# Performance work log

Measured on AMD Instinct MI355X. Metric: run time of the kernel, lower is better.

## Reference

```python
import jax, jax.numpy as jnp
import numpy as np

EMB = 1024
HEAD = 64
RANK = 8
LRA_SCL = 2.0
LORA = 1.0


def setup_inputs() -> dict:
    key = jax.random.key(0)
    ks = jax.random.split(key, 12)
    s = 1.0 / np.sqrt(EMB)
    sr = 1.0 / np.sqrt(RANK)
    inp = {
        "batEmb": jax.random.normal(ks[0], (8, 2048, EMB), dtype=jnp.float32),
        "tokMrk": jax.random.randint(ks[1], (8, 2048), 0, 2, dtype=jnp.int32),
        # base projections, nn.Linear weight layout [out, in]
        "Wq": jax.random.uniform(ks[2], (HEAD, EMB), jnp.float32, -s, s),
        "Wk": jax.random.uniform(ks[3], (HEAD, EMB), jnp.float32, -s, s),
        "Wv": jax.random.uniform(ks[4], (HEAD, EMB), jnp.float32, -s, s),
        # LoRA: A [rank, emb], B [head, rank]. (Original inits B to zero; we
        # randomize with small scale so the LoRA path is numerically exercised.)
        "Aq": jax.random.uniform(ks[5], (RANK, EMB), jnp.float32, -s, s),
        "Bq": jax.random.uniform(ks[6], (HEAD, RANK), jnp.float32, -sr, sr) * 0.02,
        "Ak": jax.random.uniform(ks[7], (RANK, EMB), jnp.float32, -s, s),
        "Bk": jax.random.uniform(ks[8], (HEAD, RANK), jnp.float32, -sr, sr) * 0.02,
        "Av": jax.random.uniform(ks[9], (RANK, EMB), jnp.float32, -s, s),
        "Bv": jax.random.uniform(ks[10], (HEAD, RANK), jnp.float32, -sr, sr) * 0.02,
    }
    return inp


def _proj(x, W, A, B):
    # base + LoRA low-rank delta (dropout = identity in eval)
    base = jnp.einsum('bse,he->bsh', x, W)
    lora = jnp.einsum('bsr,hr->bsh', jnp.einsum('bse,re->bsr', x, A), B)
    return base + lora * (LRA_SCL * LORA)


def reference(batEmb, tokMrk, Wq, Wk, Wv, Aq, Bq, Ak, Bk, Av, Bv):
    q = _proj(batEmb, Wq, Aq, Bq)  # [B,S,H]
    k = _proj(batEmb, Wk, Ak, Bk)
    v = _proj(batEmb, Wv, Av, Bv)
    w = jnp.einsum('bqh,bkh->bqk', q, k) * (HEAD ** -0.5)  # [B,S,S]
    mask = (tokMrk == 0)[:, None, :]  # [B,1,S] over key dim
    w = jnp.where(mask, -jnp.inf, w)
    w = jax.nn.softmax(w, axis=-1)
    w = jnp.nan_to_num(w, nan=0.0)
    return jnp.einsum('bqk,bkh->bqh', w, v)
```

## Files before the change

### kernel.cpp

```cpp
#include <hip/hip_runtime.h>
#include <hip/hip_bf16.h>
#include <stdint.h>

#define EMB 1024
#define NB 8
#define SEQ 2048
#define RANK 8
#define SPLIT 4

#define BM 32
#define BK 64
#define NSTG 16
#define XBUF 8192
#define WBUF 24576

#define QSCL 0.180336880f

typedef __attribute__((ext_vector_type(8))) short bf16x8;
typedef __attribute__((ext_vector_type(4))) float f32x4;
typedef unsigned short u16;
typedef unsigned int u32;

__device__ __forceinline__ u16 f2bf(float f) {
  u32 u = __builtin_bit_cast(u32, f);
  u = (u + 0x7fffu + ((u >> 16) & 1u)) >> 16;
  return (u16)u;
}
__device__ __forceinline__ u32 pk2(float lo, float hi) {
  return (u32)f2bf(lo) | ((u32)f2bf(hi) << 16);
}
__device__ __forceinline__ u32 cvtpk(float lo, float hi) {
  __hip_bfloat162 h = __float22bfloat162_rn(make_float2(lo, hi));
  u32 u; __builtin_memcpy(&u, &h, 4); return u;
}
__device__ __forceinline__ void gll16(const void* g, void* l) {
  __builtin_amdgcn_global_load_lds(
      (const __attribute__((address_space(1))) unsigned int*)g,
      (__attribute__((address_space(3))) unsigned int*)l, 16, 0, 0);
}

#define PBAR()   asm volatile("s_barrier" ::: "memory")
#define WAITV(n) asm volatile("s_waitcnt vmcnt(" #n ")" ::: "memory")

__global__ __launch_bounds__(256) void fold_k(
    const float* __restrict__ Wq, const float* __restrict__ Wk, const float* __restrict__ Wv,
    const float* __restrict__ Aq, const float* __restrict__ Bq,
    const float* __restrict__ Ak, const float* __restrict__ Bk,
    const float* __restrict__ Av, const float* __restrict__ Bv,
    u16* __restrict__ weff) {
  int m = blockIdx.x;
  int mat = m >> 6, h = m & 63;
  const float* W = mat == 0 ? Wq : (mat == 1 ? Wk : Wv);
  const float* A = mat == 0 ? Aq : (mat == 1 ? Ak : Av);
  const float* B = mat == 0 ? Bq : (mat == 1 ? Bk : Bv);
  float bb[RANK];
#pragma unroll
  for (int r = 0; r < RANK; r++) bb[r] = 2.0f * B[h * RANK + r];
  int e = threadIdx.x * 4;
  float4 w4 = *(const float4*)(W + h * EMB + e);
  float a0 = w4.x, a1 = w4.y, a2 = w4.z, a3 = w4.w;
#pragma unroll
  for (int r = 0; r < RANK; r++) {
    float4 av = *(const float4*)(A + r * EMB + e);
    a0 += bb[r] * av.x; a1 += bb[r] * av.y; a2 += bb[r] * av.z; a3 += bb[r] * av.w;
  }
  u16* o = weff + (size_t)m * EMB + e;
  o[0] = f2bf(a0); o[1] = f2bf(a1); o[2] = f2bf(a2); o[3] = f2bf(a3);
}

__global__ __launch_bounds__(320) void proj_k(
    const float* __restrict__ X, const u16* __restrict__ weff,
    u16* __restrict__ qws, u16* __restrict__ kws, u16* __restrict__ vws) {
  extern __shared__ __align__(16) char smem[];
  char* xsm = smem;
  char* wsm = smem + 3 * XBUF;

  int t = threadIdx.x;
  int w = t >> 6, l = t & 63;
  int rbase = blockIdx.x * BM;

  if (w >= 3) {
    int q = w - 3;
    int lr4 = l >> 4;
    int l15 = l & 15;
    int wc0 = l >> 3;
    int wkoff = ((l & 7) ^ wc0) * 8;

#define ISSUE_X(st, bufp) do {                                                 \
    _Pragma("unroll")                                                          \
    for (int i_ = 0; i_ < 4; i_++) {                                           \
      int rrel_ = q * 16 + i_ * 4 + lr4;                                       \
      int xo_ = 4 * (l15 ^ (rrel_ & 7));        \
      gll16(X + (size_t)(rbase + rrel_) * EMB + (st) * BK + xo_,               \
            (bufp) + q * 4096 + i_ * 1024);                                    \
    } } while (0)

#define ISSUE_W(st, bufp) do {                                                 \
    _Pragma("unroll")                                                          \
    for (int i_ = 0; i_ < 12; i_++) { int wj_ = q * 12 + i_;                   \
      gll16(weff + (size_t)(wj_ * 8 + wc0) * EMB + (st) * BK + wkoff,          \
            (bufp) + wj_ * 1024);                                              \
    } } while (0)

    ISSUE_W(0, wsm);
    ISSUE_X(0, xsm);
    ISSUE_X(1, xsm + XBUF);
    WAITV(4);
    PBAR();
    for (int s = 0; s < NSTG; s++) {
      if (s + 1 < NSTG) ISSUE_W(s + 1, wsm + ((s + 1) & 1) * WBUF);
      if (s + 2 < NSTG) ISSUE_X(s + 2, xsm + ((s + 2) % 3) * XBUF);
      if (s + 1 < NSTG) {
        if (s + 2 < NSTG) { WAITV(4); } else { WAITV(0); }
        PBAR();
      }
    }
#undef ISSUE_X
#undef ISSUE_W
  } else {
    int l15 = l & 15, lh = l >> 4;
    f32x4 acc[2][4];
    f32x4 zero = {0.f, 0.f, 0.f, 0.f};
#pragma unroll
    for (int rt = 0; rt < 2; rt++)
#pragma unroll
      for (int ct = 0; ct < 4; ct++) acc[rt][ct] = zero;

    for (int s = 0; s < NSTG; s++) {
      PBAR();
      const char* bx = xsm + (s % 3) * XBUF;
      const char* bw = wsm + (s & 1) * WBUF;
#pragma unroll
      for (int j = 0; j < 2; j++) {
        bf16x8 a[2];
#pragma unroll
        for (int rt = 0; rt < 2; rt++) {
          int r = rt * 16 + l15;
          int sw = (r & 7) << 4;
          const char* base = bx + r * 256;
          f32x4 lo = *(const f32x4*)(base + ((j * 128 + lh * 32) ^ sw));
          f32x4 hi = *(const f32x4*)(base + ((j * 128 + lh * 32 + 16) ^ sw));
          union { bf16x8 v; u32 u[4]; } au;
          au.u[0] = cvtpk(lo.x, lo.y); au.u[1] = cvtpk(lo.z, lo.w);
          au.u[2] = cvtpk(hi.x, hi.y); au.u[3] = cvtpk(hi.z, hi.w);
          a[rt] = au.v;
        }
        __builtin_amdgcn_s_setprio(1);
#pragma unroll
        for (int ct = 0; ct < 4; ct++) {
          int col = w * 64 + ct * 16 + l15;
          bf16x8 bf = *(const bf16x8*)(bw + col * 128 +
                                       ((j * 64 + lh * 16) ^ ((col & 7) << 4)));
#pragma unroll
          for (int rt = 0; rt < 2; rt++)
            acc[rt][ct] = __builtin_amdgcn_mfma_f32_16x16x32_bf16(a[rt], bf, acc[rt][ct], 0, 0, 0);
        }
        __builtin_amdgcn_s_setprio(0);
      }
    }

#pragma unroll
    for (int rt = 0; rt < 2; rt++)
#pragma unroll
      for (int ct = 0; ct < 4; ct++) {
        int c = w * 64 + ct * 16 + l15;
#pragma unroll
        for (int r = 0; r < 4; r++) {
          int rr = rbase + rt * 16 + lh * 4 + r;
          float av = acc[rt][ct][r];
          if (c < 64) av *= QSCL;
          u16 v = f2bf(av);
          if (c < 64) {
            qws[(size_t)rr * 64 + c] = v;
          } else if (c < 128) {
            kws[(size_t)rr * 64 + (c - 64)] = v;
          } else {
            int bb = rr >> 11, tok = rr & 2047;
            vws[((size_t)(bb * 64 + (c - 128))) * SEQ + tok] = v;
          }
        }
      }
  }
}

__global__ __launch_bounds__(256) void attn_k(
    const u16* __restrict__ qws, const u16* __restrict__ kws, const u16* __restrict__ vws,
    const int* __restrict__ mrk,
    float* __restrict__ po, float* __restrict__ pmp, float* __restrict__ plp) {
  __shared__ __align__(16) u16 ks[2 * 4096];
  __shared__ __align__(16) u16 vt[2 * 4096];
  __shared__ __align__(16) u16 ps[4 * 1024];
  __shared__ __align__(16) float mska[SEQ / SPLIT];

  int b = blockIdx.y;
  int z = blockIdx.z;
  int q0 = blockIdx.x * 64;
  int t = threadIdx.x;
  int w = t >> 6, l = t & 63;
  int l15 = l & 15, lh = l >> 4;

  int srow = t >> 3;
  int ssw = (((t & 7) << 4) ^ ((srow & 7) << 4)) >> 1;
  char* ksb = (char*)ks + w * 1024;
  char* vtb = (char*)vt + w * 1024;

  const u16* qp = qws + ((size_t)(b * SEQ + q0 + w * 16 + l15)) * 64 + lh * 8;
  bf16x8 qb0 = *(const bf16x8*)qp;
  bf16x8 qb1 = *(const bf16x8*)(qp + 32);

  f32x4 o[4];
  f32x4 zero = {0.f, 0.f, 0.f, 0.f};
#pragma unroll
  for (int ht = 0; ht < 4; ht++) o[ht] = zero;
  float mrow = -30000.0f, lrow = 0.f;

  int swz = (l15 & 7) << 4;
  int koffA = ((lh << 4) ^ swz) >> 1;
  int koffB = ((64 | (lh << 4)) ^ swz) >> 1;
  u16* psw = ps + w * 1024 + l15 * 64;

  const int NC = SEQ / 64 / SPLIT;
  int kk0 = z * (SEQ / SPLIT);

#define STAGE_KV(buf, kk)                                                          \
  do {                                                                             \
    gll16(kws + ((size_t)(b * SEQ + (kk) + srow)) * 64 + ssw,                      \
          ksb + (buf) * 8192);                                                     \
    gll16(kws + ((size_t)(b * SEQ + (kk) + srow + 32)) * 64 + ssw,                 \
          ksb + (buf) * 8192 + 4096);                                              \
    gll16(vws + ((size_t)(b * 64 + srow)) * SEQ + (kk) + ssw,                      \
          vtb + (buf) * 8192);                                                     \
    gll16(vws + ((size_t)(b * 64 + srow + 32)) * SEQ + (kk) + ssw,                 \
          vtb + (buf) * 8192 + 4096);                                              \
  } while (0)

  STAGE_KV(0, kk0);
  {
    int2 mi2 = *(const int2*)(mrk + b * SEQ + kk0 + t * 2);
    mska[t * 2]     = mi2.x ? 0.0f : -INFINITY;
    mska[t * 2 + 1] = mi2.y ? 0.0f : -INFINITY;
  }
  __syncthreads();

  int cur = 0;
  for (int kc = 0; kc < NC; kc++) {
    int kk = kk0 + kc * 64;
    if (kc + 1 < NC) STAGE_KV(cur ^ 1, kk + 64);

    const u16* kb = ks + cur * 4096;
    f32x4 sa[4];
    __builtin_amdgcn_s_setprio(1);
#pragma unroll
    for (int nt = 0; nt < 4; nt++) {
      const u16* kr = kb + (nt * 16 + l15) * 64;
      bf16x8 k0 = *(const bf16x8*)(kr + koffA);
      bf16x8 k1 = *(const bf16x8*)(kr + koffB);
      f32x4 s = zero;
      s = __builtin_amdgcn_mfma_f32_16x16x32_bf16(k0, qb0, s, 0, 0, 0);
      s = __builtin_amdgcn_mfma_f32_16x16x32_bf16(k1, qb1, s, 0, 0, 0);
      sa[nt] = s;
    }
    __builtin_amdgcn_s_setprio(0);

    const u16* vbb = vt + cur * 4096;
    bf16x8 vb[4][2];
#pragma unroll
    for (int ht = 0; ht < 4; ht++) {
      const u16* vr = vbb + (ht * 16 + l15) * 64;
      vb[ht][0] = *(const bf16x8*)(vr + koffA);
      vb[ht][1] = *(const bf16x8*)(vr + koffB);
    }

#pragma unroll
    for (int nt = 0; nt < 4; nt++) {
      f32x4 km = *(const f32x4*)&mska[kc * 64 + nt * 16 + lh * 4];
      sa[nt][0] += km[0];
      sa[nt][1] += km[1];
      sa[nt][2] += km[2];
      sa[nt][3] += km[3];
    }
    float t0 = fmaxf(fmaxf(sa[0][0], sa[0][1]), fmaxf(sa[0][2], sa[0][3]));
    float t1 = fmaxf(fmaxf(sa[1][0], sa[1][1]), fmaxf(sa[1][2], sa[1][3]));
    float t2 = fmaxf(fmaxf(sa[2][0], sa[2][1]), fmaxf(sa[2][2], sa[2][3]));
    float t3 = fmaxf(fmaxf(sa[3][0], sa[3][1]), fmaxf(sa[3][2], sa[3][3]));
    float tm = fmaxf(fmaxf(t0, t1), fmaxf(t2, t3));
    tm = fmaxf(tm, __shfl_xor(tm, 16));
    tm = fmaxf(tm, __shfl_xor(tm, 32));

    if (!__all(tm <= mrow + 11.5f)) {
      float nm = fmaxf(mrow, tm);
      float alpha = exp2f(mrow - nm);
      mrow = nm;
      lrow *= alpha;
      float a0 = __shfl(alpha, lh * 4 + 0);
      float a1 = __shfl(alpha, lh * 4 + 1);
      float a2 = __shfl(alpha, lh * 4 + 2);
      float a3 = __shfl(alpha, lh * 4 + 3);
#pragma unroll
      for (int ht = 0; ht < 4; ht++) {
        o[ht][0] *= a0; o[ht][1] *= a1; o[ht][2] *= a2; o[ht][3] *= a3;
      }
    }

    float ts = 0.f;
#pragma unroll
    for (int nt = 0; nt < 4; nt++) {
#pragma unroll
      for (int r = 0; r < 4; r++) {
        float p = exp2f(sa[nt][r] - mrow);
        sa[nt][r] = p;
        ts += p;
      }
    }
    ts += __shfl_xor(ts, 16);
    ts += __shfl_xor(ts, 32);
    lrow += ts;

#pragma unroll
    for (int nt = 0; nt < 4; nt++) {
      u32 plo = pk2(sa[nt][0], sa[nt][1]);
      u32 phi = pk2(sa[nt][2], sa[nt][3]);
      *(uint2*)&psw[(((nt * 32 + lh * 8) ^ swz) >> 1)] = make_uint2(plo, phi);
    }
    bf16x8 ap0 = *(const bf16x8*)(psw + koffA);
    bf16x8 ap1 = *(const bf16x8*)(psw + koffB);

    __builtin_amdgcn_s_setprio(1);
#pragma unroll
    for (int ht = 0; ht < 4; ht++) {
      o[ht] = __builtin_amdgcn_mfma_f32_16x16x32_bf16(ap0, vb[ht][0], o[ht], 0, 0, 0);
      o[ht] = __builtin_amdgcn_mfma_f32_16x16x32_bf16(ap1, vb[ht][1], o[ht], 0, 0, 0);
    }
    __builtin_amdgcn_s_setprio(0);
    __syncthreads();
    cur ^= 1;
  }
#undef STAGE_KV

#pragma unroll
  for (int r = 0; r < 4; r++) {
    int rr = q0 + w * 16 + lh * 4 + r;
    float* pob = po + ((size_t)z * NB * SEQ + (size_t)b * SEQ + rr) * 64;
#pragma unroll
    for (int ht = 0; ht < 4; ht++) pob[ht * 16 + l15] = o[ht][r];
  }
  if (lh == 0) {
    int rr = q0 + w * 16 + l15;
    pmp[(size_t)z * NB * SEQ + (size_t)b * SEQ + rr] = mrow;
    plp[(size_t)z * NB * SEQ + (size_t)b * SEQ + rr] = lrow;
  }
}

__global__ __launch_bounds__(256) void merge_k(
    const float* __restrict__ po, const float* __restrict__ pmp,
    const float* __restrict__ plp, float* __restrict__ out) {
  int tid = threadIdx.x;
  int row = blockIdx.x * 32 + (tid >> 3);
  int c8 = (tid & 7) * 8;
  const int RT = NB * SEQ;

  float m[SPLIT], lv[SPLIT];
  float M = -INFINITY;
#pragma unroll
  for (int s = 0; s < SPLIT; s++) {
    m[s] = pmp[(size_t)s * RT + row];
    lv[s] = plp[(size_t)s * RT + row];
    M = fmaxf(M, m[s]);
  }
  float o8[8];
#pragma unroll
  for (int j = 0; j < 8; j++) o8[j] = 0.f;
  float L = 0.f;
  if (M != -INFINITY) {
#pragma unroll
    for (int s = 0; s < SPLIT; s++) {
      float ws = exp2f(m[s] - M);
      L += ws * lv[s];
      const float* p = po + ((size_t)s * RT + row) * 64 + c8;
#pragma unroll
      for (int j = 0; j < 8; j++) o8[j] += ws * p[j];
    }
  }
  float inv = (L > 0.f) ? 1.0f / L : 0.f;
  float* op = out + (size_t)row * 64 + c8;
#pragma unroll
  for (int j = 0; j < 8; j++) op[j] = o8[j] * inv;
}

extern "C" void kernel_launch(void* const* d_in, const int* in_sizes, int n_in,
                              void* d_out, int out_size, void* d_ws, size_t ws_size,
                              hipStream_t stream) {
  const float* X   = (const float*)d_in[0];
  const int*   mrk = (const int*)d_in[1];
  const float* Wq  = (const float*)d_in[2];
  const float* Wk  = (const float*)d_in[3];
  const float* Wv  = (const float*)d_in[4];
  const float* Aq  = (const float*)d_in[5];
  const float* Bq  = (const float*)d_in[6];
  const float* Ak  = (const float*)d_in[7];
  const float* Bk  = (const float*)d_in[8];
  const float* Av  = (const float*)d_in[9];
  const float* Bv  = (const float*)d_in[10];

  u16* weff = (u16*)d_ws;
  u16* qws  = (u16*)((char*)d_ws + (512 << 10));
  u16* kws  = qws + (size_t)16384 * 64;
  u16* vws  = kws + (size_t)16384 * 64;
  float* po  = (float*)((char*)d_ws + ((size_t)6656 << 10));
  float* pmp = po + (size_t)SPLIT * 16384 * 64;
  float* plp = pmp + (size_t)SPLIT * 16384;

  (void)hipFuncSetAttribute((const void*)proj_k,
                            hipFuncAttributeMaxDynamicSharedMemorySize,
                            3 * XBUF + 2 * WBUF);

  fold_k<<<192, 256, 0, stream>>>(Wq, Wk, Wv, Aq, Bq, Ak, Bk, Av, Bv, weff);
  proj_k<<<512, 320, 3 * XBUF + 2 * WBUF, stream>>>(X, weff, qws, kws, vws);
  attn_k<<<dim3(32, 8, SPLIT), 256, 0, stream>>>(qws, kws, vws, mrk, po, pmp, plp);
  merge_k<<<512, 256, 0, stream>>>(po, pmp, plp, (float*)d_out);
}
```

Baseline: 59.78 us.

## Split producer warps into dedicated X and weight loaders with deeper X ring

The projection kernel's two producer waves previously each loaded half of both the activation and the weight tiles in lockstep. Now one wave streams activation tiles through a four-deep ring, prefetching three stages ahead, and the other wave streams weight tiles through the double buffer. This decouples the large-latency X stream from the weight stream so X can run further ahead. It costs an extra shared-memory buffer, and the weight wave now waits fully on each stage, which may serialize its own loads.

Result: slower. 61.83 us (+3.4%).

```diff
diff --git a/kernel.cpp b/kernel.cpp
--- a/kernel.cpp
+++ b/kernel.cpp
@@ -13,6 +13,7 @@
 #define NSTG 16
 #define XBUF 8192
 #define WBUF 24576
+#define NXB 4
 
 #define QSCL 0.180336880f
 
@@ -73,50 +74,62 @@
     u16* __restrict__ qws, u16* __restrict__ kws, u16* __restrict__ vws) {
   extern __shared__ __align__(16) char smem[];
   char* xsm = smem;
-  char* wsm = smem + 3 * XBUF;
+  char* wsm = smem + NXB * XBUF;
 
   int t = threadIdx.x;
   int w = t >> 6, l = t & 63;
   int rbase = blockIdx.x * BM;
 
-  if (w >= 3) {
-    int q = w - 3;
+  if (w == 3) {
     int lr4 = l >> 4;
     int l15 = l & 15;
+
+#define ISSX(st) do {                                                          \
+    char* bufp_ = xsm + ((st) % NXB) * XBUF;                                   \
+    _Pragma("unroll")                                                          \
+    for (int i_ = 0; i_ < 8; i_++) {                                           \
+      int rrel_ = i_ * 4 + lr4;                                                \
+      int xo_ = 4 * (l15 ^ (rrel_ & 7));        \
+      gll16(X + (size_t)(rbase + rrel_) * EMB + (st) * BK + xo_,               \
+            bufp_ + i_ * 1024);                                                \
+    } } while (0)
+
+    ISSX(0); ISSX(1); ISSX(2);
+    WAITV(16);
+    PBAR();
+    for (int s = 0; s < NSTG - 1; s++) {
+      if (s + 3 < NSTG) {
+        ISSX(s + 3);
+        WAITV(16);
+      } else if (s + 2 < NSTG) {
+        WAITV(8);
+      } else {
+        WAITV(0);
+      }
+      PBAR();
+    }
+#undef ISSX
+  } else if (w == 4) {
     int wc0 = l >> 3;
     int wkoff = ((l & 7) ^ wc0) * 8;
 
-#define ISSUE_X(st, bufp) do {                                                 \
+#define ISSW(st) do {                                                          \
+    char* bufp_ = wsm + ((st) & 1) * WBUF;                                     \
     _Pragma("unroll")                                                          \
-    for (int i_ = 0; i_ < 4; i_++) {                                           \
-      int rrel_ = q * 16 + i_ * 4 + lr4;                                       \
-      int xo_ = 4 * (l15 ^ (rrel_ & 7));        \
-      gll16(X + (size_t)(rbase + rrel_) * EMB + (st) * BK + xo_,               \
-            (bufp) + q * 4096 + i_ * 1024);                                    \
+    for (int i_ = 0; i_ < 24; i_++) {                                          \
+      gll16(weff + (size_t)(i_ * 8 + wc0) * EMB + (st) * BK + wkoff,           \
+            bufp_ + i_ * 1024);                                                \
     } } while (0)
 
-#define ISSUE_W(st, bufp) do {                                                 \
-    _Pragma("unroll")                                                          \
-    for (int i_ = 0; i_ < 12; i_++) { int wj_ = q * 12 + i_;                   \
-      gll16(weff + (size_t)(wj_ * 8 + wc0) * EMB + (st) * BK + wkoff,          \
-            (bufp) + wj_ * 1024);                                              \
-    } } while (0)
-
-    ISSUE_W(0, wsm);
-    ISSUE_X(0, xsm);
-    ISSUE_X(1, xsm + XBUF);
-    WAITV(4);
+    ISSW(0);
+    WAITV(0);
     PBAR();
-    for (int s = 0; s < NSTG; s++) {
-      if (s + 1 < NSTG) ISSUE_W(s + 1, wsm + ((s + 1) & 1) * WBUF);
-      if (s + 2 < NSTG) ISSUE_X(s + 2, xsm + ((s + 2) % 3) * XBUF);
-      if (s + 1 < NSTG) {
-        if (s + 2 < NSTG) { WAITV(4); } else { WAITV(0); }
-        PBAR();
-      }
-    }
-#undef ISSUE_X
-#undef ISSUE_W
+    for (int s = 0; s < NSTG - 1; s++) {
+      ISSW(s + 1);
+      WAITV(0);
+      PBAR();
+    }
+#undef ISSW
   } else {
     int l15 = l & 15, lh = l >> 4;
     f32x4 acc[2][4];
@@ -128,7 +141,7 @@
 
     for (int s = 0; s < NSTG; s++) {
       PBAR();
-      const char* bx = xsm + (s % 3) * XBUF;
+      const char* bx = xsm + (s % NXB) * XBUF;
       const char* bw = wsm + (s & 1) * WBUF;
 #pragma unroll
       for (int j = 0; j < 2; j++) {
@@ -412,10 +425,10 @@
 
   (void)hipFuncSetAttribute((const void*)proj_k,
                             hipFuncAttributeMaxDynamicSharedMemorySize,
-                            3 * XBUF + 2 * WBUF);
+                            NXB * XBUF + 2 * WBUF);
 
   fold_k<<<192, 256, 0, stream>>>(Wq, Wk, Wv, Aq, Bq, Ak, Bk, Av, Bv, weff);
-  proj_k<<<512, 320, 3 * XBUF + 2 * WBUF, stream>>>(X, weff, qws, kws, vws);
+  proj_k<<<512, 320, NXB * XBUF + 2 * WBUF, stream>>>(X, weff, qws, kws, vws);
   attn_k<<<dim3(32, 8, SPLIT), 256, 0, stream>>>(qws, kws, vws, mrk, po, pmp, plp);
   merge_k<<<512, 256, 0, stream>>>(po, pmp, plp, (float*)d_out);
 }
```
